# Performance work log

Hardware: AMD Instinct MI355X
Metric: run time of the kernel (lower is better)

## Reference

```python
import jax, jax.numpy as jnp
import numpy as np

W0 = 30.0  # SIREN omega_0
IN_DIM, HIDDEN, OUT_DIM = 32, [32, 32, 32], 3
DIMS = [IN_DIM] + HIDDEN + [OUT_DIM]
LAYER_SIZES = [DIMS[i] * DIMS[i + 1] + DIMS[i + 1] for i in range(len(DIMS) - 1)]
TOTAL_PARAMS = int(np.sum(LAYER_SIZES))  # 3267

N, S, P, PH, PHH = 96, 4096, 4096, 1024, 512


def st(x):
    # self.st = softplus(x, beta=1, threshold=20) / 6
    return jax.nn.softplus(x) / 6.0


def setup_inputs() -> dict:
    key = jax.random.key(0)
    ks = jax.random.split(key, 14)
    return {
        "x": jax.random.normal(ks[0], (N, S, IN_DIM), dtype=jnp.float32),
        "loc": 0.05 * jax.random.normal(ks[1], (N, P), dtype=jnp.float32),
        "log_scale": jnp.full((N, P), -4.0, dtype=jnp.float32),
        "h_loc": 0.05 * jax.random.normal(ks[2], (N // 16, PH), dtype=jnp.float32),
        "h_log_scale": jnp.full((N // 16, PH), -4.0, dtype=jnp.float32),
        "hh_loc": 0.05 * jax.random.normal(ks[3], (N // 96, PHH), dtype=jnp.float32),
        "hh_log_scale": jnp.full((N // 96, PHH), -4.0, dtype=jnp.float32),
        "eps": jax.random.normal(ks[4], (N, P), dtype=jnp.float32),
        "h_eps": jax.random.normal(ks[5], (N // 16, PH), dtype=jnp.float32),
        "hh_eps": jax.random.normal(ks[6], (N // 96, PHH), dtype=jnp.float32),
        "W_map": jax.random.normal(ks[7], (P, TOTAL_PARAMS), dtype=jnp.float32) / np.sqrt(P),
        "b_map": jnp.zeros((TOTAL_PARAMS,), dtype=jnp.float32),
        "h_group_idx": jax.random.randint(ks[8], (P,), 0, PH, dtype=jnp.int32),
        "hh_group_idx": jax.random.randint(ks[9], (P,), 0, PHH, dtype=jnp.int32),
    }


def reference(x, loc, log_scale, h_loc, h_log_scale, hh_loc, hh_log_scale,
              eps, h_eps, hh_eps, W_map, b_map, h_group_idx, hh_group_idx):
    n = loc.shape[0]
    # reparameterized sampling at each level of the hierarchy: loc + eps * softplus(log_scale)/6
    s = loc + eps * st(log_scale)                       # [N, P]
    hs = h_loc + h_eps * st(h_log_scale)                # [N/16, PH]
    hhs = hh_loc + hh_eps * st(hh_log_scale)            # [N/96, PHH]
    # group-gather reconstruction: expand hierarchical latents onto per-param positions
    dp_h = jnp.arange(n) // 16                          # datapoint -> h-group
    dp_hh = jnp.arange(n) // 96                         # datapoint -> hh-group
    z = s + hs[dp_h][:, h_group_idx] + hhs[dp_hh][:, hh_group_idx]  # [N, P]
    # frozen linear param_mapping: latent -> per-datapoint network params
    params = z @ W_map + b_map                          # [N, TOTAL_PARAMS]
    # per-datapoint SIREN MLP (layer_to_weight: bias first, then weights)
    h = x
    start = 0
    for i in range(len(DIMS) - 1):
        din, dout = DIMS[i], DIMS[i + 1]
        lp = params[:, start:start + din * dout + dout]
        start += din * dout + dout
        b = lp[:, :dout][:, None, :]                    # [N, 1, dout]
        W = lp[:, dout:].reshape(n, din, dout)          # [N, din, dout]
        h = jnp.einsum('nsd,nde->nse', h, W) + b
        if i < len(DIMS) - 2:
            h = jnp.sin(W0 * h)                         # Sine(w0) activation
    return h
```

## Files before the change

kernel.cpp:

```cpp
#include <hip/hip_runtime.h>
#include <hip/hip_bf16.h>
#include <math.h>

#define NN 96
#define SS 4096
#define PP 4096
#define PH 1024
#define PHH 512
#define TP 3267
#define KC_SPLIT 16
#define KCHUNK 256
#define WSTR 68
#define ZSTR 100

typedef short short8 __attribute__((ext_vector_type(8)));
typedef float float4v __attribute__((ext_vector_type(4)));

__device__ __forceinline__ float stp(float x) {
    float sp = (x > 15.0f) ? x : log1pf(expf(x));
    return sp * (1.0f / 6.0f);
}

__device__ __forceinline__ float sin_w0(float x) {
    constexpr double Cd = 30.0 / 6.283185307179586476925286766559;
    constexpr float C_hi = (float)Cd;
    constexpr float C_lo = (float)(Cd - (double)C_hi);
    float t = x * C_hi;
    float k = rintf(t);
    float r = fmaf(x, C_hi, -k);
    r = fmaf(x, C_lo, r);
    return __builtin_amdgcn_sinf(r);
}

__device__ __forceinline__ unsigned short f2bf(float f) {
    unsigned u = __float_as_uint(f);
    unsigned r = u + 0x7fffu + ((u >> 16) & 1u);
    return (unsigned short)(r >> 16);
}
__device__ __forceinline__ float bf2f(unsigned short b) {
    return __uint_as_float(((unsigned)b) << 16);
}
__device__ __forceinline__ unsigned splitpack(float v) {
    unsigned short hb = f2bf(v);
    unsigned short lb = f2bf(v - bf2f(hb));
    return (((unsigned)hb) << 16) | (unsigned)lb;
}

__global__ __launch_bounds__(256) void z_kernel(
    const float* __restrict__ loc, const float* __restrict__ log_scale,
    const float* __restrict__ h_loc, const float* __restrict__ h_ls,
    const float* __restrict__ hh_loc, const float* __restrict__ hh_ls,
    const float* __restrict__ eps, const float* __restrict__ h_eps,
    const float* __restrict__ hh_eps,
    const int* __restrict__ h_gi, const int* __restrict__ hh_gi,
    unsigned* __restrict__ z32)
{
    int t = blockIdx.x * 256 + threadIdx.x;
    int p = t & (PP - 1);
    int n = t >> 12;
    int idx = n * PP + p;
    float s = loc[idx] + eps[idx] * stp(log_scale[idx]);
    int g  = h_gi[p];
    int gh = (n >> 4) * PH + g;
    float hs = h_loc[gh] + h_eps[gh] * stp(h_ls[gh]);
    int gg = hh_gi[p];
    float hhs = hh_loc[gg] + hh_eps[gg] * stp(hh_ls[gg]);
    z32[idx] = splitpack(s + hs + hhs);
}

#define MT(ACC, mt)                                                       \
    {                                                                     \
        short8 Ah, Al;                                                    \
        _Pragma("unroll")                                                 \
        for (int i = 0; i < 8; ++i) {                                     \
            int kl = ((i >> 2) << 4) + q4 + (i & 3);                      \
            unsigned u = zt[kl * ZSTR + (mt) * 16 + e];                   \
            Ah[i] = (short)(u >> 16);                                     \
            Al[i] = (short)(u & 0xffffu);                                 \
        }                                                                 \
        ACC = __builtin_amdgcn_mfma_f32_16x16x32_bf16(Ah, Bh, ACC, 0, 0, 0); \
        ACC = __builtin_amdgcn_mfma_f32_16x16x32_bf16(Al, Bh, ACC, 0, 0, 0); \
        ACC = __builtin_amdgcn_mfma_f32_16x16x32_bf16(Ah, Bl, ACC, 0, 0, 0); \
    }

__global__ __launch_bounds__(256, 3) void gemm_kernel(
    const float* __restrict__ Wm, const unsigned* __restrict__ z32,
    float* __restrict__ partials)
{
    int b  = blockIdx.x;
    int kc = b & 15;
    int jt = b >> 4;
    int tid = threadIdx.x;
    int wave = tid >> 6;
    int lane = tid & 63;
    int e  = lane & 15;
    int q4 = (lane >> 4) << 2;
    int j0 = (jt < 51) ? jt * 64 : (TP - 64);
    int j  = j0 + wave * 16 + e;
    int k0 = kc * KCHUNK;

    __shared__ float    wt[32 * WSTR];
    __shared__ unsigned zt[32 * ZSTR];

    float4v acc0 = {0,0,0,0}, acc1 = {0,0,0,0}, acc2 = {0,0,0,0};
    float4v acc3 = {0,0,0,0}, acc4 = {0,0,0,0}, acc5 = {0,0,0,0};

    int wrow = tid >> 3, wcol = tid & 7;
    int sm   = tid >> 1, skh = (tid & 1) << 4;

#pragma unroll 1
    for (int ks = 0; ks < KCHUNK / 32; ++ks) {
        int kb = k0 + ks * 32;

        float wv[8];
        const float* wsrc = Wm + (size_t)(kb + wrow) * TP + j0 + wcol;
#pragma unroll
        for (int u = 0; u < 8; ++u) wv[u] = wsrc[u * 8];
        unsigned zv[16];
        if (tid < 192) {
            const unsigned* zsrc = z32 + (size_t)sm * PP + kb + skh;
#pragma unroll
            for (int u = 0; u < 4; ++u)
                *(uint4*)(zv + u * 4) = *(const uint4*)(zsrc + u * 4);
        }

        __syncthreads();

#pragma unroll
        for (int u = 0; u < 8; ++u) wt[wrow * WSTR + wcol + u * 8] = wv[u];
        if (tid < 192) {
#pragma unroll
            for (int kk = 0; kk < 16; ++kk) zt[(skh + kk) * ZSTR + sm] = zv[kk];
        }

        __syncthreads();

        short8 Bh, Bl;
#pragma unroll
        for (int i = 0; i < 8; ++i) {
            int kl = ((i >> 2) << 4) + q4 + (i & 3);
            float w = wt[kl * WSTR + wave * 16 + e];
            unsigned short hb = f2bf(w);
            Bh[i] = (short)hb;
            Bl[i] = (short)f2bf(w - bf2f(hb));
        }

        MT(acc0, 0) MT(acc1, 1) MT(acc2, 2)
        MT(acc3, 3) MT(acc4, 4) MT(acc5, 5)
    }

    float* pp = partials + (size_t)(kc * NN) * TP + j;
#pragma unroll
    for (int r = 0; r < 4; ++r) pp[(size_t)(q4 + r) * TP]      = acc0[r];
#pragma unroll
    for (int r = 0; r < 4; ++r) pp[(size_t)(16 + q4 + r) * TP] = acc1[r];
#pragma unroll
    for (int r = 0; r < 4; ++r) pp[(size_t)(32 + q4 + r) * TP] = acc2[r];
#pragma unroll
    for (int r = 0; r < 4; ++r) pp[(size_t)(48 + q4 + r) * TP] = acc3[r];
#pragma unroll
    for (int r = 0; r < 4; ++r) pp[(size_t)(64 + q4 + r) * TP] = acc4[r];
#pragma unroll
    for (int r = 0; r < 4; ++r) pp[(size_t)(80 + q4 + r) * TP] = acc5[r];
}

__global__ __launch_bounds__(256) void reduce_kernel(
    const float* __restrict__ partials, const float* __restrict__ b_map,
    float* __restrict__ params)
{
    int t = blockIdx.x * 256 + threadIdx.x;
    if (t >= NN * TP) return;
    int j = t % TP;
    int n = t / TP;
    float a = b_map[j];
#pragma unroll
    for (int kc = 0; kc < KC_SPLIT; ++kc)
        a += partials[((size_t)(kc * NN + n)) * TP + j];
    params[(size_t)n * TP + j] = a;
}

#define TSTRIDE 18

#define PRELOAD_HALF(lp, off, BH, BL)                                   \
    {                                                                   \
        _Pragma("unroll")                                               \
        for (int i = 0; i < 8; ++i) {                                   \
            int k = ((i >> 2) << 4) + q4 + (i & 3);                     \
            float w = (lp)[32 + k * 32 + e + (off)];                    \
            unsigned short hb = f2bf(w);                                \
            BH[i] = (short)hb;                                          \
            BL[i] = (short)f2bf(w - bf2f(hb));                          \
        }                                                               \
    }

#define LOADX(M0, AH, AL)                                               \
    {                                                                   \
        const float* xr = x + ((size_t)(n * SS + (M0) + e)) * 32;       \
        float4 xa = *(const float4*)(xr + q4);                          \
        float4 xb = *(const float4*)(xr + 16 + q4);                     \
        float xv[8] = {xa.x, xa.y, xa.z, xa.w, xb.x, xb.y, xb.z, xb.w}; \
        _Pragma("unroll")                                               \
        for (int i = 0; i < 8; ++i) {                                   \
            unsigned short hb = f2bf(xv[i]);                            \
            AH[i] = (short)hb;                                          \
            AL[i] = (short)f2bf(xv[i] - bf2f(hb));                      \
        }                                                               \
    }

#define LAYER2(BH0, BL0, BH1, BL1, B0, B1)                              \
    {                                                                   \
        float4v pa0 = (float4v){B0, B0, B0, B0};                        \
        float4v pa1 = (float4v){B1, B1, B1, B1};                        \
        float4v pb0 = (float4v){B0, B0, B0, B0};                        \
        float4v pb1 = (float4v){B1, B1, B1, B1};                        \
        pa0 = __builtin_amdgcn_mfma_f32_16x16x32_bf16(Ahi, BH0, pa0, 0, 0, 0); \
        pb0 = __builtin_amdgcn_mfma_f32_16x16x32_bf16(Chi, BH0, pb0, 0, 0, 0); \
        pa0 = __builtin_amdgcn_mfma_f32_16x16x32_bf16(Alo, BH0, pa0, 0, 0, 0); \
        pb0 = __builtin_amdgcn_mfma_f32_16x16x32_bf16(Clo, BH0, pb0, 0, 0, 0); \
        pa0 = __builtin_amdgcn_mfma_f32_16x16x32_bf16(Ahi, BL0, pa0, 0, 0, 0); \
        pb0 = __builtin_amdgcn_mfma_f32_16x16x32_bf16(Chi, BL0, pb0, 0, 0, 0); \
        pa1 = __builtin_amdgcn_mfma_f32_16x16x32_bf16(Ahi, BH1, pa1, 0, 0, 0); \
        pb1 = __builtin_amdgcn_mfma_f32_16x16x32_bf16(Chi, BH1, pb1, 0, 0, 0); \
        pa1 = __builtin_amdgcn_mfma_f32_16x16x32_bf16(Alo, BH1, pa1, 0, 0, 0); \
        pb1 = __builtin_amdgcn_mfma_f32_16x16x32_bf16(Clo, BH1, pb1, 0, 0, 0); \
        pa1 = __builtin_amdgcn_mfma_f32_16x16x32_bf16(Ahi, BL1, pa1, 0, 0, 0); \
        pb1 = __builtin_amdgcn_mfma_f32_16x16x32_bf16(Chi, BL1, pb1, 0, 0, 0); \
        unsigned k0 = splitpack(sin_w0(pa0[0]));                        \
        unsigned k1 = splitpack(sin_w0(pa0[1]));                        \
        unsigned k2 = splitpack(sin_w0(pa0[2]));                        \
        unsigned k3 = splitpack(sin_w0(pa0[3]));                        \
        unsigned k4 = splitpack(sin_w0(pa1[0]));                        \
        unsigned k5 = splitpack(sin_w0(pa1[1]));                        \
        unsigned k6 = splitpack(sin_w0(pa1[2]));                        \
        unsigned k7 = splitpack(sin_w0(pa1[3]));                        \
        *(uint2*)(tpA + e * TSTRIDE + q4)            = make_uint2(k0, k1); \
        *(uint2*)(tpA + e * TSTRIDE + q4 + 2)        = make_uint2(k2, k3); \
        *(uint2*)(tpA + (e + 16) * TSTRIDE + q4)     = make_uint2(k4, k5); \
        *(uint2*)(tpA + (e + 16) * TSTRIDE + q4 + 2) = make_uint2(k6, k7); \
        unsigned m0_ = splitpack(sin_w0(pb0[0]));                       \
        unsigned m1_ = splitpack(sin_w0(pb0[1]));                       \
        unsigned m2_ = splitpack(sin_w0(pb0[2]));                       \
        unsigned m3_ = splitpack(sin_w0(pb0[3]));                       \
        unsigned m4_ = splitpack(sin_w0(pb1[0]));                       \
        unsigned m5_ = splitpack(sin_w0(pb1[1]));                       \
        unsigned m6_ = splitpack(sin_w0(pb1[2]));                       \
        unsigned m7_ = splitpack(sin_w0(pb1[3]));                       \
        *(uint2*)(tpB + e * TSTRIDE + q4)            = make_uint2(m0_, m1_); \
        *(uint2*)(tpB + e * TSTRIDE + q4 + 2)        = make_uint2(m2_, m3_); \
        *(uint2*)(tpB + (e + 16) * TSTRIDE + q4)     = make_uint2(m4_, m5_); \
        *(uint2*)(tpB + (e + 16) * TSTRIDE + q4 + 2) = make_uint2(m6_, m7_); \
        asm volatile("s_waitcnt lgkmcnt(0)" ::: "memory");              \
        __builtin_amdgcn_sched_barrier(0);                              \
        _Pragma("unroll")                                               \
        for (int i = 0; i < 8; ++i) {                                   \
            int k = ((i >> 2) << 4) + q4 + (i & 3);                     \
            unsigned u = tpA[k * TSTRIDE + e];                          \
            Ahi[i] = (short)(u >> 16);                                  \
            Alo[i] = (short)(u & 0xffffu);                              \
            unsigned v = tpB[k * TSTRIDE + e];                          \
            Chi[i] = (short)(v >> 16);                                  \
            Clo[i] = (short)(v & 0xffffu);                              \
        }                                                               \
    }

__global__ __launch_bounds__(256, 3) void mlp_kernel(
    const float* __restrict__ x, const float* __restrict__ params,
    float* __restrict__ out)
{
    int b = blockIdx.x;
    int n = b >> 4;
    int chunk = b & 15;
    int tid = threadIdx.x;
    int wave = tid >> 6;
    int lane = tid & 63;
    int e  = lane & 15;
    int q4 = (lane >> 4) << 2;

    __shared__ unsigned tiles[4][2][32 * TSTRIDE];
    unsigned* tpA = tiles[wave][0];
    unsigned* tpB = tiles[wave][1];

    const float* pr = params + (size_t)n * TP;

    short8 B0h0, B0l0, B0h1, B0l1;
    short8 B1h0, B1l0, B1h1, B1l1;
    short8 B2h0, B2l0, B2h1, B2l1;
    short8 BFh, BFl;
    float b0_0, b0_1, b1_0, b1_1, b2_0, b2_1, bF;

    { const float* lp = pr;            b0_0 = lp[e]; b0_1 = lp[e + 16];
      PRELOAD_HALF(lp, 0, B0h0, B0l0)  PRELOAD_HALF(lp, 16, B0h1, B0l1) }
    { const float* lp = pr + 1056;     b1_0 = lp[e]; b1_1 = lp[e + 16];
      PRELOAD_HALF(lp, 0, B1h0, B1l0)  PRELOAD_HALF(lp, 16, B1h1, B1l1) }
    { const float* lp = pr + 2112;     b2_0 = lp[e]; b2_1 = lp[e + 16];
      PRELOAD_HALF(lp, 0, B2h0, B2l0)  PRELOAD_HALF(lp, 16, B2h1, B2l1) }
    {
        const float* lpf = pr + 3168;
        bF = (e < 3) ? lpf[e] : 0.0f;
#pragma unroll
        for (int i = 0; i < 8; ++i) {
            int k = ((i >> 2) << 4) + q4 + (i & 3);
            float w = (e < 3) ? lpf[3 + k * 3 + e] : 0.0f;
            unsigned short hb = f2bf(w);
            BFh[i] = (short)hb;
            BFl[i] = (short)f2bf(w - bf2f(hb));
        }
    }

    int p0 = chunk * 256 + wave * 64;

#pragma unroll 1
    for (int it = 0; it < 2; ++it) {
        int m0 = p0 + it * 32;

        short8 Ahi, Alo, Chi, Clo;
        LOADX(m0, Ahi, Alo)
        LOADX(m0 + 16, Chi, Clo)

        LAYER2(B0h0, B0l0, B0h1, B0l1, b0_0, b0_1)
        LAYER2(B1h0, B1l0, B1h1, B1l1, b1_0, b1_1)
        LAYER2(B2h0, B2l0, B2h1, B2l1, b2_0, b2_1)

        float4v fA = (float4v){bF, bF, bF, bF};
        float4v fB = (float4v){bF, bF, bF, bF};
        fA = __builtin_amdgcn_mfma_f32_16x16x32_bf16(Ahi, BFh, fA, 0, 0, 0);
        fB = __builtin_amdgcn_mfma_f32_16x16x32_bf16(Chi, BFh, fB, 0, 0, 0);
        fA = __builtin_amdgcn_mfma_f32_16x16x32_bf16(Alo, BFh, fA, 0, 0, 0);
        fB = __builtin_amdgcn_mfma_f32_16x16x32_bf16(Clo, BFh, fB, 0, 0, 0);
        fA = __builtin_amdgcn_mfma_f32_16x16x32_bf16(Ahi, BFl, fA, 0, 0, 0);
        fB = __builtin_amdgcn_mfma_f32_16x16x32_bf16(Chi, BFl, fB, 0, 0, 0);

        if (e < 3) {
#pragma unroll
            for (int r = 0; r < 4; ++r)
                out[((size_t)n * SS + m0 + q4 + r) * 3 + e] = fA[r];
#pragma unroll
            for (int r = 0; r < 4; ++r)
                out[((size_t)n * SS + m0 + 16 + q4 + r) * 3 + e] = fB[r];
        }
    }
}

extern "C" void kernel_launch(void* const* d_in, const int* in_sizes, int n_in,
                              void* d_out, int out_size, void* d_ws, size_t ws_size,
                              hipStream_t stream)
{
    const float* x        = (const float*)d_in[0];
    const float* loc      = (const float*)d_in[1];
    const float* log_sc   = (const float*)d_in[2];
    const float* h_loc    = (const float*)d_in[3];
    const float* h_ls     = (const float*)d_in[4];
    const float* hh_loc   = (const float*)d_in[5];
    const float* hh_ls    = (const float*)d_in[6];
    const float* eps      = (const float*)d_in[7];
    const float* h_eps    = (const float*)d_in[8];
    const float* hh_eps   = (const float*)d_in[9];
    const float* W_map    = (const float*)d_in[10];
    const float* b_map    = (const float*)d_in[11];
    const int*   h_gi     = (const int*)d_in[12];
    const int*   hh_gi    = (const int*)d_in[13];
    float* out = (float*)d_out;

    unsigned* z32  = (unsigned*)d_ws;
    float* partials = (float*)(z32 + (size_t)NN * PP);
    float* params   = partials + (size_t)KC_SPLIT * NN * TP;

    z_kernel<<<(NN * PP) / 256, 256, 0, stream>>>(
        loc, log_sc, h_loc, h_ls, hh_loc, hh_ls, eps, h_eps, hh_eps,
        h_gi, hh_gi, z32);

    gemm_kernel<<<52 * 16, 256, 0, stream>>>(W_map, z32, partials);

    reduce_kernel<<<(NN * TP + 255) / 256, 256, 0, stream>>>(partials, b_map, params);

    mlp_kernel<<<96 * 16, 256, 0, stream>>>(x, params, out);
}
```

Measured before the change: 64.32 us.

## Compute transposed MLP layers so activations stay in registers without LDS

The per-datapoint SIREN layers are recast as W^T·H^T, with the weights as the MFMA A operand and the activations as the B operand. The output fragment of each layer then lines up with the next layer's B-operand layout, so the LDS round trip, waitcnt and sched barrier between layers go away. Each wave now processes 16 rows per iteration over four iterations instead of 32 rows over two. Occupancy in launch_bounds rises from 3 to 4. This trades LDS traffic and its sync for less ILP per iteration, since one MFMA chain replaces two interleaved ones.

After: 73.31 us. 14.0% more time.

```diff
diff --git a/kernel.cpp b/kernel.cpp
--- a/kernel.cpp
+++ b/kernel.cpp
@@ -45,6 +45,14 @@
     unsigned short lb = f2bf(v - bf2f(hb));
     return (((unsigned)hb) << 16) | (unsigned)lb;
 }
+
+#define SPLIT2I(V, VH, VL, I)                                           \
+    {                                                                   \
+        float _v = (V);                                                 \
+        unsigned short _hb = f2bf(_v);                                  \
+        VH[I] = (short)_hb;                                             \
+        VL[I] = (short)f2bf(_v - bf2f(_hb));                            \
+    }
 
 __global__ __launch_bounds__(256) void z_kernel(
     const float* __restrict__ loc, const float* __restrict__ log_scale,
@@ -179,91 +187,37 @@
     params[(size_t)n * TP + j] = a;
 }
 
-#define TSTRIDE 18
 
 #define PRELOAD_HALF(lp, off, BH, BL)                                   \
     {                                                                   \
         _Pragma("unroll")                                               \
         for (int i = 0; i < 8; ++i) {                                   \
             int k = ((i >> 2) << 4) + q4 + (i & 3);                     \
-            float w = (lp)[32 + k * 32 + e + (off)];                    \
-            unsigned short hb = f2bf(w);                                \
-            BH[i] = (short)hb;                                          \
-            BL[i] = (short)f2bf(w - bf2f(hb));                          \
+            SPLIT2I((lp)[32 + k * 32 + e + (off)], BH, BL, i)           \
         }                                                               \
     }
 
-#define LOADX(M0, AH, AL)                                               \
+#define SLAYER(WH0, WL0, WH1, WL1, B0V, B1V)                            \
     {                                                                   \
-        const float* xr = x + ((size_t)(n * SS + (M0) + e)) * 32;       \
-        float4 xa = *(const float4*)(xr + q4);                          \
-        float4 xb = *(const float4*)(xr + 16 + q4);                     \
-        float xv[8] = {xa.x, xa.y, xa.z, xa.w, xb.x, xb.y, xb.z, xb.w}; \
-        _Pragma("unroll")                                               \
-        for (int i = 0; i < 8; ++i) {                                   \
-            unsigned short hb = f2bf(xv[i]);                            \
-            AH[i] = (short)hb;                                          \
-            AL[i] = (short)f2bf(xv[i] - bf2f(hb));                      \
-        }                                                               \
-    }
-
-#define LAYER2(BH0, BL0, BH1, BL1, B0, B1)                              \
-    {                                                                   \
-        float4v pa0 = (float4v){B0, B0, B0, B0};                        \
-        float4v pa1 = (float4v){B1, B1, B1, B1};                        \
-        float4v pb0 = (float4v){B0, B0, B0, B0};                        \
-        float4v pb1 = (float4v){B1, B1, B1, B1};                        \
-        pa0 = __builtin_amdgcn_mfma_f32_16x16x32_bf16(Ahi, BH0, pa0, 0, 0, 0); \
-        pb0 = __builtin_amdgcn_mfma_f32_16x16x32_bf16(Chi, BH0, pb0, 0, 0, 0); \
-        pa0 = __builtin_amdgcn_mfma_f32_16x16x32_bf16(Alo, BH0, pa0, 0, 0, 0); \
-        pb0 = __builtin_amdgcn_mfma_f32_16x16x32_bf16(Clo, BH0, pb0, 0, 0, 0); \
-        pa0 = __builtin_amdgcn_mfma_f32_16x16x32_bf16(Ahi, BL0, pa0, 0, 0, 0); \
-        pb0 = __builtin_amdgcn_mfma_f32_16x16x32_bf16(Chi, BL0, pb0, 0, 0, 0); \
-        pa1 = __builtin_amdgcn_mfma_f32_16x16x32_bf16(Ahi, BH1, pa1, 0, 0, 0); \
-        pb1 = __builtin_amdgcn_mfma_f32_16x16x32_bf16(Chi, BH1, pb1, 0, 0, 0); \
-        pa1 = __builtin_amdgcn_mfma_f32_16x16x32_bf16(Alo, BH1, pa1, 0, 0, 0); \
-        pb1 = __builtin_amdgcn_mfma_f32_16x16x32_bf16(Clo, BH1, pb1, 0, 0, 0); \
-        pa1 = __builtin_amdgcn_mfma_f32_16x16x32_bf16(Ahi, BL1, pa1, 0, 0, 0); \
-        pb1 = __builtin_amdgcn_mfma_f32_16x16x32_bf16(Chi, BL1, pb1, 0, 0, 0); \
-        unsigned k0 = splitpack(sin_w0(pa0[0]));                        \
-        unsigned k1 = splitpack(sin_w0(pa0[1]));                        \
-        unsigned k2 = splitpack(sin_w0(pa0[2]));                        \
-        unsigned k3 = splitpack(sin_w0(pa0[3]));                        \
-        unsigned k4 = splitpack(sin_w0(pa1[0]));                        \
-        unsigned k5 = splitpack(sin_w0(pa1[1]));                        \
-        unsigned k6 = splitpack(sin_w0(pa1[2]));                        \
-        unsigned k7 = splitpack(sin_w0(pa1[3]));                        \
-        *(uint2*)(tpA + e * TSTRIDE + q4)            = make_uint2(k0, k1); \
-        *(uint2*)(tpA + e * TSTRIDE + q4 + 2)        = make_uint2(k2, k3); \
-        *(uint2*)(tpA + (e + 16) * TSTRIDE + q4)     = make_uint2(k4, k5); \
-        *(uint2*)(tpA + (e + 16) * TSTRIDE + q4 + 2) = make_uint2(k6, k7); \
-        unsigned m0_ = splitpack(sin_w0(pb0[0]));                       \
-        unsigned m1_ = splitpack(sin_w0(pb0[1]));                       \
-        unsigned m2_ = splitpack(sin_w0(pb0[2]));                       \
-        unsigned m3_ = splitpack(sin_w0(pb0[3]));                       \
-        unsigned m4_ = splitpack(sin_w0(pb1[0]));                       \
-        unsigned m5_ = splitpack(sin_w0(pb1[1]));                       \
-        unsigned m6_ = splitpack(sin_w0(pb1[2]));                       \
-        unsigned m7_ = splitpack(sin_w0(pb1[3]));                       \
-        *(uint2*)(tpB + e * TSTRIDE + q4)            = make_uint2(m0_, m1_); \
-        *(uint2*)(tpB + e * TSTRIDE + q4 + 2)        = make_uint2(m2_, m3_); \
-        *(uint2*)(tpB + (e + 16) * TSTRIDE + q4)     = make_uint2(m4_, m5_); \
-        *(uint2*)(tpB + (e + 16) * TSTRIDE + q4 + 2) = make_uint2(m6_, m7_); \
-        asm volatile("s_waitcnt lgkmcnt(0)" ::: "memory");              \
-        __builtin_amdgcn_sched_barrier(0);                              \
-        _Pragma("unroll")                                               \
-        for (int i = 0; i < 8; ++i) {                                   \
-            int k = ((i >> 2) << 4) + q4 + (i & 3);                     \
-            unsigned u = tpA[k * TSTRIDE + e];                          \
-            Ahi[i] = (short)(u >> 16);                                  \
-            Alo[i] = (short)(u & 0xffffu);                              \
-            unsigned v = tpB[k * TSTRIDE + e];                          \
-            Chi[i] = (short)(v >> 16);                                  \
-            Clo[i] = (short)(v & 0xffffu);                              \
-        }                                                               \
-    }
-
-__global__ __launch_bounds__(256, 3) void mlp_kernel(
+        float4v a0 = (float4v){B0V.x, B0V.y, B0V.z, B0V.w};             \
+        float4v a1 = (float4v){B1V.x, B1V.y, B1V.z, B1V.w};             \
+        a0 = __builtin_amdgcn_mfma_f32_16x16x32_bf16(WH0, Hh, a0, 0, 0, 0); \
+        a1 = __builtin_amdgcn_mfma_f32_16x16x32_bf16(WH1, Hh, a1, 0, 0, 0); \
+        a0 = __builtin_amdgcn_mfma_f32_16x16x32_bf16(WH0, Hl, a0, 0, 0, 0); \
+        a1 = __builtin_amdgcn_mfma_f32_16x16x32_bf16(WH1, Hl, a1, 0, 0, 0); \
+        a0 = __builtin_amdgcn_mfma_f32_16x16x32_bf16(WL0, Hh, a0, 0, 0, 0); \
+        a1 = __builtin_amdgcn_mfma_f32_16x16x32_bf16(WL1, Hh, a1, 0, 0, 0); \
+        SPLIT2I(sin_w0(a0[0]), Hh, Hl, 0)                               \
+        SPLIT2I(sin_w0(a0[1]), Hh, Hl, 1)                               \
+        SPLIT2I(sin_w0(a0[2]), Hh, Hl, 2)                               \
+        SPLIT2I(sin_w0(a0[3]), Hh, Hl, 3)                               \
+        SPLIT2I(sin_w0(a1[0]), Hh, Hl, 4)                               \
+        SPLIT2I(sin_w0(a1[1]), Hh, Hl, 5)                               \
+        SPLIT2I(sin_w0(a1[2]), Hh, Hl, 6)                               \
+        SPLIT2I(sin_w0(a1[3]), Hh, Hl, 7)                               \
+    }
+
+__global__ __launch_bounds__(256, 4) void mlp_kernel(
     const float* __restrict__ x, const float* __restrict__ params,
     float* __restrict__ out)
 {
@@ -276,67 +230,71 @@
     int e  = lane & 15;
     int q4 = (lane >> 4) << 2;
 
-    __shared__ unsigned tiles[4][2][32 * TSTRIDE];
-    unsigned* tpA = tiles[wave][0];
-    unsigned* tpB = tiles[wave][1];
-
     const float* pr = params + (size_t)n * TP;
 
-    short8 B0h0, B0l0, B0h1, B0l1;
-    short8 B1h0, B1l0, B1h1, B1l1;
-    short8 B2h0, B2l0, B2h1, B2l1;
-    short8 BFh, BFl;
-    float b0_0, b0_1, b1_0, b1_1, b2_0, b2_1, bF;
-
-    { const float* lp = pr;            b0_0 = lp[e]; b0_1 = lp[e + 16];
-      PRELOAD_HALF(lp, 0, B0h0, B0l0)  PRELOAD_HALF(lp, 16, B0h1, B0l1) }
-    { const float* lp = pr + 1056;     b1_0 = lp[e]; b1_1 = lp[e + 16];
-      PRELOAD_HALF(lp, 0, B1h0, B1l0)  PRELOAD_HALF(lp, 16, B1h1, B1l1) }
-    { const float* lp = pr + 2112;     b2_0 = lp[e]; b2_1 = lp[e + 16];
-      PRELOAD_HALF(lp, 0, B2h0, B2l0)  PRELOAD_HALF(lp, 16, B2h1, B2l1) }
+    short8 W0h0, W0l0, W0h1, W0l1;
+    short8 W1h0, W1l0, W1h1, W1l1;
+    short8 W2h0, W2l0, W2h1, W2l1;
+    short8 WFh, WFl;
+    float4 b0v, b1v, b2v, b0w, b1w, b2w, bFv;
+
+    { const float* lp = pr;
+      b0v = *(const float4*)(lp + q4); b0w = *(const float4*)(lp + 16 + q4);
+      PRELOAD_HALF(lp, 0, W0h0, W0l0)  PRELOAD_HALF(lp, 16, W0h1, W0l1) }
+    { const float* lp = pr + 1056;
+      b1v = *(const float4*)(lp + q4); b1w = *(const float4*)(lp + 16 + q4);
+      PRELOAD_HALF(lp, 0, W1h0, W1l0)  PRELOAD_HALF(lp, 16, W1h1, W1l1) }
+    { const float* lp = pr + 2112;
+      b2v = *(const float4*)(lp + q4); b2w = *(const float4*)(lp + 16 + q4);
+      PRELOAD_HALF(lp, 0, W2h0, W2l0)  PRELOAD_HALF(lp, 16, W2h1, W2l1) }
     {
         const float* lpf = pr + 3168;
-        bF = (e < 3) ? lpf[e] : 0.0f;
+        float4 bt = *(const float4*)(lpf + q4);
+        bFv.x = (q4 + 0 < 3) ? bt.x : 0.0f;
+        bFv.y = (q4 + 1 < 3) ? bt.y : 0.0f;
+        bFv.z = (q4 + 2 < 3) ? bt.z : 0.0f;
+        bFv.w = 0.0f;
 #pragma unroll
         for (int i = 0; i < 8; ++i) {
             int k = ((i >> 2) << 4) + q4 + (i & 3);
             float w = (e < 3) ? lpf[3 + k * 3 + e] : 0.0f;
-            unsigned short hb = f2bf(w);
-            BFh[i] = (short)hb;
-            BFl[i] = (short)f2bf(w - bf2f(hb));
+            SPLIT2I(w, WFh, WFl, i)
         }
     }
 
     int p0 = chunk * 256 + wave * 64;
 
 #pragma unroll 1
-    for (int it = 0; it < 2; ++it) {
-        int m0 = p0 + it * 32;
-
-        short8 Ahi, Alo, Chi, Clo;
-        LOADX(m0, Ahi, Alo)
-        LOADX(m0 + 16, Chi, Clo)
-
-        LAYER2(B0h0, B0l0, B0h1, B0l1, b0_0, b0_1)
-        LAYER2(B1h0, B1l0, B1h1, B1l1, b1_0, b1_1)
-        LAYER2(B2h0, B2l0, B2h1, B2l1, b2_0, b2_1)
-
-        float4v fA = (float4v){bF, bF, bF, bF};
-        float4v fB = (float4v){bF, bF, bF, bF};
-        fA = __builtin_amdgcn_mfma_f32_16x16x32_bf16(Ahi, BFh, fA, 0, 0, 0);
-        fB = __builtin_amdgcn_mfma_f32_16x16x32_bf16(Chi, BFh, fB, 0, 0, 0);
-        fA = __builtin_amdgcn_mfma_f32_16x16x32_bf16(Alo, BFh, fA, 0, 0, 0);
-        fB = __builtin_amdgcn_mfma_f32_16x16x32_bf16(Clo, BFh, fB, 0, 0, 0);
-        fA = __builtin_amdgcn_mfma_f32_16x16x32_bf16(Ahi, BFl, fA, 0, 0, 0);
-        fB = __builtin_amdgcn_mfma_f32_16x16x32_bf16(Chi, BFl, fB, 0, 0, 0);
-
-        if (e < 3) {
-#pragma unroll
-            for (int r = 0; r < 4; ++r)
-                out[((size_t)n * SS + m0 + q4 + r) * 3 + e] = fA[r];
-#pragma unroll
-            for (int r = 0; r < 4; ++r)
-                out[((size_t)n * SS + m0 + 16 + q4 + r) * 3 + e] = fB[r];
+    for (int it = 0; it < 4; ++it) {
+        int m0 = p0 + it * 16;
+
+        short8 Hh, Hl;
+        {
+            const float* xr = x + ((size_t)(n * SS + m0 + e)) * 32;
+            float4 xa = *(const float4*)(xr + q4);
+            float4 xb = *(const float4*)(xr + 16 + q4);
+            SPLIT2I(xa.x, Hh, Hl, 0)
+            SPLIT2I(xa.y, Hh, Hl, 1)
+            SPLIT2I(xa.z, Hh, Hl, 2)
+            SPLIT2I(xa.w, Hh, Hl, 3)
+            SPLIT2I(xb.x, Hh, Hl, 4)
+            SPLIT2I(xb.y, Hh, Hl, 5)
+            SPLIT2I(xb.z, Hh, Hl, 6)
+            SPLIT2I(xb.w, Hh, Hl, 7)
+        }
+
+        SLAYER(W0h0, W0l0, W0h1, W0l1, b0v, b0w)
+        SLAYER(W1h0, W1l0, W1h1, W1l1, b1v, b1w)
+        SLAYER(W2h0, W2l0, W2h1, W2l1, b2v, b2w)
+
+        float4v fA = (float4v){bFv.x, bFv.y, bFv.z, bFv.w};
+        fA = __builtin_amdgcn_mfma_f32_16x16x32_bf16(WFh, Hh, fA, 0, 0, 0);
+        fA = __builtin_amdgcn_mfma_f32_16x16x32_bf16(WFh, Hl, fA, 0, 0, 0);
+        fA = __builtin_amdgcn_mfma_f32_16x16x32_bf16(WFl, Hh, fA, 0, 0, 0);
+
+        if (q4 == 0) {
+            float* op = out + ((size_t)n * SS + m0 + e) * 3;
+            op[0] = fA[0]; op[1] = fA[1]; op[2] = fA[2];
         }
     }
 }
```
